# Performance work log

Hardware: AMD Instinct MI355X
Metric: run time of the kernel (lower is better)

Reference implementation:

```python
import jax, jax.numpy as jnp
import numpy as np
import math

B, S, D, H, R = 4, 2048, 2048, 16, 16
HD = D // H

def setup_inputs() -> dict:
    key = jax.random.key(0)
    ks = jax.random.split(key, 16)
    x = jax.random.normal(ks[0], (B, S, D), dtype=jnp.float32)
    # causal mask: 1 where attendable, 0 where masked (mask==0 -> -1e9)
    mask = jnp.tril(jnp.ones((S, S), dtype=jnp.int32))[None, None, :, :]
    def lin(k):
        return jax.random.normal(k, (D, D), dtype=jnp.float32) / math.sqrt(D)
    def lora(ka, kb):
        A = jax.random.normal(ka, (R, D), dtype=jnp.float32) / math.sqrt(D)
        Bm = jnp.zeros((D, R), dtype=jnp.float32)  # standard LoRA init: B = 0
        return A, Bm
    Aq, Bq = lora(ks[1], ks[2]); Ak, Bk = lora(ks[3], ks[4])
    Av, Bv = lora(ks[5], ks[6]); Ao, Bo = lora(ks[7], ks[8])
    return {"x": x, "mask": mask,
            "Wq": lin(ks[9]), "Aq": Aq, "Bq": Bq,
            "Wk": lin(ks[10]), "Ak": Ak, "Bk": Bk,
            "Wv": lin(ks[11]), "Av": Av, "Bv": Bv,
            "Wo": lin(ks[12]), "Ao": Ao, "Bo": Bo}

def _lora_linear(x, W, A, Bm):
    # y = x @ W^T + (x @ A^T) @ B^T   (LoRA-augmented linear, no bias)
    return x @ W.T + (x @ A.T) @ Bm.T

def reference(x, mask, Wq, Aq, Bq, Wk, Ak, Bk, Wv, Av, Bv, Wo, Ao, Bo):
    b, s, d = x.shape
    def heads(t):
        return t.reshape(b, s, H, HD).transpose(0, 2, 1, 3)  # [B,H,S,HD]
    Q = heads(_lora_linear(x, Wq, Aq, Bq))
    K = heads(_lora_linear(x, Wk, Ak, Bk))
    V = heads(_lora_linear(x, Wv, Av, Bv))
    attn = jnp.einsum('bhqd,bhkd->bhqk', Q, K) / math.sqrt(HD)
    attn = jnp.where(mask == 0, jnp.float32(-1e9), attn)
    attn = jax.nn.softmax(attn, axis=-1)
    out = jnp.einsum('bhqk,bhkd->bhqd', attn, V)  # [B,H,S,HD]
    out = out.transpose(0, 2, 1, 3).reshape(b, s, d)
    return _lora_linear(out, Wo, Ao, Bo)
```

## Files before the change

### kernel.cpp

```cpp
#include <hip/hip_runtime.h>
#include <hip/hip_bf16.h>
#include <stdint.h>


#define L2E 1.4426950408889634f
#define SMSCALE 0.08838834764831845f
#define NEGBIG -3.0e38f

typedef __attribute__((ext_vector_type(4))) float f32x4;
typedef __attribute__((ext_vector_type(16))) float f32x16;
typedef __attribute__((ext_vector_type(8))) __bf16 bfrag;

#if __has_builtin(__builtin_amdgcn_exp2f)
#define EXP2 __builtin_amdgcn_exp2f
#else
#define EXP2 exp2f
#endif

#define DRAIN_VM                                      \
  do {                                                \
    asm volatile("s_waitcnt vmcnt(0)" ::: "memory");  \
    __builtin_amdgcn_sched_barrier(0);                \
  } while (0)

static __device__ __forceinline__ unsigned short f2bf(float f) {
  union { float f; unsigned u; } v; v.f = f;
  unsigned r = v.u + 0x7FFFu + ((v.u >> 16) & 1u);
  return (unsigned short)(r >> 16);
}

static __device__ __forceinline__ void gload16(const void* g, void* l) {
  __builtin_amdgcn_global_load_lds(
      (const __attribute__((address_space(1))) void*)g,
      (__attribute__((address_space(3))) void*)l, 16, 0, 0);
}

__global__ __launch_bounds__(256) void k_fold(const float* __restrict__ W,
                                              const float* __restrict__ A,
                                              const float* __restrict__ Bm,
                                              unsigned short* __restrict__ out) {
  const int n = blockIdx.x;
  const int k0 = threadIdx.x * 8;
  const float* wr = W + (size_t)n * 2048 + k0;
  float acc[8];
#pragma unroll
  for (int j = 0; j < 8; ++j) acc[j] = wr[j];
#pragma unroll 4
  for (int r = 0; r < 16; ++r) {
    float b = Bm[n * 16 + r];
    const float* ar = A + (size_t)r * 2048 + k0;
#pragma unroll
    for (int j = 0; j < 8; ++j) acc[j] = fmaf(b, ar[j], acc[j]);
  }
  unsigned short o[8];
#pragma unroll
  for (int j = 0; j < 8; ++j) o[j] = f2bf(acc[j]);
  *(uint4*)(out + (size_t)n * 2048 + k0) = *(const uint4*)o;
}

__global__ __launch_bounds__(256) void k_cvt(const float* __restrict__ in,
                                             unsigned short* __restrict__ out) {
  const size_t i = ((size_t)blockIdx.x * 256 + threadIdx.x) * 8;
  unsigned short o[8];
#pragma unroll
  for (int j = 0; j < 8; ++j) o[j] = f2bf(in[i + j]);
  *(uint4*)(out + i) = *(const uint4*)o;
}

template <int MODE>
__global__ __launch_bounds__(512, 2) void k_gemm2(const unsigned short* __restrict__ A,
                                                  const unsigned short* __restrict__ Bw,
                                                  void* __restrict__ Cout, float scale) {
  __shared__ __align__(16) unsigned char lds[131072];
  unsigned char* Al = lds;
  unsigned char* Bl = lds + 65536;
  const int tid = threadIdx.x, ln = tid & 63;
  const int w = tid >> 6, g = ln >> 4, cc = ln & 15;
  const int wm = w >> 2, wn = w & 3;
  const int bid = blockIdx.x;
  const int wg = (bid & 7) * 32 + (bid >> 3);
  const int m0 = (wg >> 3) * 256, n0 = (wg & 7) * 256;

  int soff[2], sdst[2];
#pragma unroll
  for (int i = 0; i < 2; ++i) {
    int cid = i * 512 + tid, r = cid >> 2, p = cid & 3;
    int sc = p ^ ((r >> 1) & 3);
    soff[i] = r * 2048 + sc * 8;
    sdst[i] = cid * 16;
  }
  int aro[8], bro[4];
#pragma unroll
  for (int fm = 0; fm < 8; ++fm) {
    int r = wm * 128 + fm * 16 + cc;
    aro[fm] = r * 64 + ((g ^ ((r >> 1) & 3)) << 4);
  }
#pragma unroll
  for (int fn = 0; fn < 4; ++fn) {
    int r = wn * 64 + fn * 16 + cc;
    bro[fn] = r * 64 + ((g ^ ((r >> 1) & 3)) << 4);
  }

#define STAGE_A(b, kt, h)                                                   \
  do {                                                                      \
    _Pragma("unroll")                                                       \
    for (int i = 0; i < 2; ++i)                                             \
      gload16(A + (size_t)m0 * 2048 + soff[i] + (kt) + (h) * 32,            \
              Al + (b) * 32768 + (h) * 16384 + sdst[i]);                    \
  } while (0)
#define STAGE_B(b, kt, h)                                                   \
  do {                                                                      \
    _Pragma("unroll")                                                       \
    for (int i = 0; i < 2; ++i)                                             \
      gload16(Bw + (size_t)n0 * 2048 + soff[i] + (kt) + (h) * 32,           \
              Bl + (b) * 32768 + (h) * 16384 + sdst[i]);                    \
  } while (0)

  f32x4 acc[8][4] = {};

  STAGE_A(0, 0, 0); STAGE_B(0, 0, 0);
  STAGE_A(0, 0, 1); STAGE_B(0, 0, 1);
  STAGE_A(1, 64, 0); STAGE_B(1, 64, 0);
  asm volatile("s_waitcnt vmcnt(8)" ::: "memory");
  __builtin_amdgcn_s_barrier();
  __builtin_amdgcn_sched_barrier(0);

  for (int T = 0; T < 32; ++T) {
    const int buf = T & 1;
    const unsigned char* Ab = Al + buf * 32768;
    const unsigned char* Bb = Bl + buf * 32768;
#pragma unroll
    for (int ks = 0; ks < 2; ++ks) {
      bfrag af[8], bf[4];
#pragma unroll
      for (int fm = 0; fm < 8; ++fm)
        af[fm] = *(const bfrag*)(Ab + ks * 16384 + aro[fm]);
#pragma unroll
      for (int j = 0; j < 2; ++j)
        bf[j] = *(const bfrag*)(Bb + ks * 16384 + bro[j]);
      __builtin_amdgcn_sched_barrier(0);
      __builtin_amdgcn_s_barrier();
      __builtin_amdgcn_sched_barrier(0);
      __builtin_amdgcn_s_setprio(1);
#pragma unroll
      for (int fm = 0; fm < 8; ++fm)
#pragma unroll
        for (int j = 0; j < 2; ++j)
          acc[fm][j] = __builtin_amdgcn_mfma_f32_16x16x32_bf16(af[fm], bf[j],
                                                               acc[fm][j], 0, 0, 0);
      __builtin_amdgcn_s_setprio(0);
      __builtin_amdgcn_sched_barrier(0);
#pragma unroll
      for (int j = 0; j < 2; ++j)
        bf[2 + j] = *(const bfrag*)(Bb + ks * 16384 + bro[2 + j]);
      if (ks == 0) {
        if (T + 1 < 32) {
          STAGE_A(buf ^ 1, (T + 1) * 64, 1);
          STAGE_B(buf ^ 1, (T + 1) * 64, 1);
        }
        __builtin_amdgcn_sched_barrier(0);
        if (T < 31) asm volatile("s_waitcnt vmcnt(8)" ::: "memory");
        else        asm volatile("s_waitcnt vmcnt(0)" ::: "memory");
      } else {
        if (T + 2 < 32) {
          STAGE_A(buf, (T + 2) * 64, 0);
          STAGE_B(buf, (T + 2) * 64, 0);
        }
        __builtin_amdgcn_sched_barrier(0);
        if (T < 30) asm volatile("s_waitcnt vmcnt(8)" ::: "memory");
        else        asm volatile("s_waitcnt vmcnt(0)" ::: "memory");
      }
      __builtin_amdgcn_s_barrier();
      __builtin_amdgcn_sched_barrier(0);
      __builtin_amdgcn_s_setprio(1);
#pragma unroll
      for (int fm = 0; fm < 8; ++fm)
#pragma unroll
        for (int j = 0; j < 2; ++j)
          acc[fm][2 + j] = __builtin_amdgcn_mfma_f32_16x16x32_bf16(af[fm], bf[2 + j],
                                                                   acc[fm][2 + j], 0, 0, 0);
      __builtin_amdgcn_s_setprio(0);
      __builtin_amdgcn_sched_barrier(0);
    }
  }
#undef STAGE_A
#undef STAGE_B

#pragma unroll
  for (int fm = 0; fm < 8; ++fm)
#pragma unroll
    for (int fn = 0; fn < 4; ++fn)
#pragma unroll
      for (int r = 0; r < 4; ++r) {
        int row = m0 + wm * 128 + fm * 16 + g * 4 + r;
        int col = n0 + wn * 64 + fn * 16 + cc;
        float v = acc[fm][fn][r];
        if (MODE == 0) {
          int b = row >> 11, s = row & 2047, h = col >> 7, hd = col & 127;
          ((unsigned short*)Cout)[(((size_t)b * 16 + h) * 2048 + s) * 128 + hd] =
              f2bf(v * scale);
        } else if (MODE == 2) {
          int b = row >> 11, s = row & 2047, h = col >> 7, hd = col & 127;
          ((unsigned short*)Cout)[(((size_t)b * 16 + h) * 128 + hd) * 2048 + s] =
              f2bf(v);
        } else {
          ((float*)Cout)[(size_t)row * 2048 + col] = v;
        }
      }
}

__global__ __launch_bounds__(512) void k_attn(const unsigned short* __restrict__ Q,
                                              const unsigned short* __restrict__ K,
                                              const unsigned short* __restrict__ Vt,
                                              unsigned short* __restrict__ O) {
  __shared__ __align__(16) unsigned char lds[65536];
  const int tid = threadIdx.x;
  const int ln = tid & 63, w = tid >> 6;
  const int l31 = ln & 31, hi = ln >> 5;
  const int rk = l31 & 15;
  const int bx = blockIdx.x;
  const int qb = 7 - (bx >> 6);
  const int bh = bx & 63;
  const int q0 = qb * 256;
  const size_t base = (size_t)bh * 2048 * 128;
  const unsigned short* Qb = Q + base;
  const unsigned short* Kb = K + base;
  const unsigned short* Vb = Vt + base;

  const int qw0 = q0 + w * 32;
  const int qg = qw0 + l31;

  bfrag qf[8];
#pragma unroll
  for (int dc = 0; dc < 8; ++dc)
    qf[dc] = *(const bfrag*)(Qb + (size_t)qg * 128 + dc * 16 + hi * 8);

  f32x16 o[4] = {};
  float m_r = NEGBIG, l_r = 0.f;

  const int nt = q0 / 64 + 4;

  auto stage = [&](int buf, int k0) {
    unsigned char* Kt = lds + buf * 32768;
    unsigned char* Vl = Kt + 16384;
#pragma unroll
    for (int i = 0; i < 2; ++i) {
      int cid = i * 512 + tid;
      int row = cid >> 4, p = cid & 15, sc = p ^ (row & 15);
      gload16(Kb + (size_t)(k0 + row) * 128 + sc * 8, Kt + cid * 16);
    }
#pragma unroll
    for (int i = 0; i < 2; ++i) {
      int cid = i * 512 + tid;
      int row = cid >> 4, p = cid & 15, sc = p ^ (row & 15);
      int d = (sc >> 3) * 64 + row;
      gload16(Vb + (size_t)d * 2048 + k0 + (sc & 7) * 8, Vl + cid * 16);
    }
  };

  stage(0, 0);
  DRAIN_VM;
  __syncthreads();
  int buf = 0;

  for (int t = 0; t < nt; ++t) {
    const int k0 = t * 64;
    if (t + 1 < nt) stage(buf ^ 1, k0 + 64);

    if (k0 <= qw0 + 31) {
      const unsigned char* Kt = lds + buf * 32768;
      const unsigned char* Vl = Kt + 16384;

      f32x16 s0 = {}, s1 = {};
#pragma unroll
      for (int dc = 0; dc < 8; ++dc) {
        int c = dc * 2 + hi;
        bfrag ka = *(const bfrag*)(Kt + (size_t)l31 * 256 + ((c ^ rk) << 4));
        bfrag kb2 = *(const bfrag*)(Kt + (size_t)(32 + l31) * 256 + ((c ^ rk) << 4));
        s0 = __builtin_amdgcn_mfma_f32_32x32x16_bf16(ka, qf[dc], s0, 0, 0, 0);
        s1 = __builtin_amdgcn_mfma_f32_32x32x16_bf16(kb2, qf[dc], s1, 0, 0, 0);
      }

      if (k0 + 63 > qw0) {
#pragma unroll
        for (int r = 0; r < 16; ++r) {
          int ko = (r & 3) + 8 * (r >> 2) + 4 * hi;
          if (k0 + ko > qg) s0[r] = NEGBIG;
          if (k0 + 32 + ko > qg) s1[r] = NEGBIG;
        }
      }

      float pmax = s0[0];
#pragma unroll
      for (int r = 1; r < 16; ++r) pmax = fmaxf(pmax, s0[r]);
#pragma unroll
      for (int r = 0; r < 16; ++r) pmax = fmaxf(pmax, s1[r]);
      pmax = fmaxf(pmax, __shfl_xor(pmax, 32));

      if (!__all(pmax - m_r <= 12.f)) {
        float mn = fmaxf(m_r, pmax);
        float al = EXP2(m_r - mn);
        l_r *= al;
#pragma unroll
        for (int db = 0; db < 4; ++db)
#pragma unroll
          for (int r = 0; r < 16; ++r) o[db][r] *= al;
        m_r = mn;
      }

      unsigned qd0[8], qd1[8];
      float rs = 0.f;
#pragma unroll
      for (int s = 0; s < 4; ++s) {
        float p0 = EXP2(s0[4 * s + 0] - m_r), p1 = EXP2(s0[4 * s + 1] - m_r);
        float p2 = EXP2(s0[4 * s + 2] - m_r), p3 = EXP2(s0[4 * s + 3] - m_r);
        rs += (p0 + p1) + (p2 + p3);
        qd0[2 * s] = (unsigned)f2bf(p0) | ((unsigned)f2bf(p1) << 16);
        qd0[2 * s + 1] = (unsigned)f2bf(p2) | ((unsigned)f2bf(p3) << 16);
      }
#pragma unroll
      for (int s = 0; s < 4; ++s) {
        float p0 = EXP2(s1[4 * s + 0] - m_r), p1 = EXP2(s1[4 * s + 1] - m_r);
        float p2 = EXP2(s1[4 * s + 2] - m_r), p3 = EXP2(s1[4 * s + 3] - m_r);
        rs += (p0 + p1) + (p2 + p3);
        qd1[2 * s] = (unsigned)f2bf(p0) | ((unsigned)f2bf(p1) << 16);
        qd1[2 * s + 1] = (unsigned)f2bf(p2) | ((unsigned)f2bf(p3) << 16);
      }
      rs += __shfl_xor(rs, 32);
      l_r += rs;

#define PVSTEP(QD, B0, KC)                                                    \
  do {                                                                        \
    unsigned e0 = QD[B0], e1 = QD[B0 + 1], x0 = QD[B0 + 2], x1 = QD[B0 + 3];  \
    unsigned kp0 = hi ? x0 : e0, kp1 = hi ? x1 : e1;                          \
    unsigned sd0 = hi ? e0 : x0, sd1 = hi ? e1 : x1;                          \
    unsigned rc0 = (unsigned)__shfl_xor((int)sd0, 32);                        \
    unsigned rc1 = (unsigned)__shfl_xor((int)sd1, 32);                        \
    unsigned pw[4];                                                           \
    pw[0] = hi ? rc0 : kp0; pw[1] = hi ? rc1 : kp1;                           \
    pw[2] = hi ? kp0 : rc0; pw[3] = hi ? kp1 : rc1;                           \
    bfrag pf = *(bfrag*)pw;                                                   \
    _Pragma("unroll")                                                         \
    for (int db = 0; db < 4; ++db) {                                          \
      int c = (db >> 1) * 8 + KC * 2 + hi;                                    \
      bfrag vf = *(const bfrag*)(Vl + (size_t)((db & 1) * 32 + l31) * 256 +   \
                                 ((c ^ rk) << 4));                            \
      o[db] = __builtin_amdgcn_mfma_f32_32x32x16_bf16(vf, pf, o[db], 0, 0, 0);\
    }                                                                         \
  } while (0)

      PVSTEP(qd0, 0, 0);
      PVSTEP(qd0, 4, 1);
      PVSTEP(qd1, 0, 2);
      PVSTEP(qd1, 4, 3);
#undef PVSTEP
    }
    DRAIN_VM;
    __syncthreads();
    buf ^= 1;
  }

  float invl = 1.0f / l_r;
  const int b_ = bh >> 4, h_ = bh & 15;
#pragma unroll
  for (int ph = 0; ph < 2; ++ph) {
    if ((w >> 2) == ph) {
      unsigned char* ep = lds + (w & 3) * 8704;
#pragma unroll
      for (int db = 0; db < 4; ++db)
#pragma unroll
        for (int s = 0; s < 4; ++s) {
          int d0 = db * 32 + 8 * s + 4 * hi;
          float v0 = o[db][4 * s] * invl, v1 = o[db][4 * s + 1] * invl;
          float v2 = o[db][4 * s + 2] * invl, v3 = o[db][4 * s + 3] * invl;
          uint2 pw;
          pw.x = (unsigned)f2bf(v0) | ((unsigned)f2bf(v1) << 16);
          pw.y = (unsigned)f2bf(v2) | ((unsigned)f2bf(v3) << 16);
          *(uint2*)(ep + l31 * 272 + d0 * 2) = pw;
        }
    }
    __syncthreads();
    if ((w >> 2) == ph) {
      const unsigned char* ep = lds + (w & 3) * 8704;
#pragma unroll
      for (int i = 0; i < 8; ++i) {
        int cid = i * 64 + ln;
        int q = cid >> 4, ch = cid & 15;
        uint4 val = *(const uint4*)(ep + q * 272 + ch * 16);
        *(uint4*)(O + ((size_t)(b_ * 2048 + q0 + w * 32 + q)) * 2048 +
                  h_ * 128 + ch * 8) = val;
      }
    }
    __syncthreads();
  }
}

extern "C" void kernel_launch(void* const* d_in, const int* in_sizes, int n_in,
                              void* d_out, int out_size, void* d_ws, size_t ws_size,
                              hipStream_t stream) {
  (void)in_sizes; (void)n_in; (void)out_size; (void)ws_size;
  const float* x  = (const float*)d_in[0];
  const float* Wq = (const float*)d_in[2];
  const float* Aq = (const float*)d_in[3];
  const float* Bq = (const float*)d_in[4];
  const float* Wk = (const float*)d_in[5];
  const float* Ak = (const float*)d_in[6];
  const float* Bk = (const float*)d_in[7];
  const float* Wv = (const float*)d_in[8];
  const float* Av = (const float*)d_in[9];
  const float* Bv = (const float*)d_in[10];
  const float* Wo = (const float*)d_in[11];
  const float* Ao = (const float*)d_in[12];
  const float* Bo = (const float*)d_in[13];

  char* ws = (char*)d_ws;
  unsigned short* xbf = (unsigned short*)ws;
  unsigned short* Wqe = (unsigned short*)(ws + (size_t)33554432);
  unsigned short* Wke = Wqe + 2048 * 2048;
  unsigned short* Wve = Wke + 2048 * 2048;
  unsigned short* Woe = Wve + 2048 * 2048;
  unsigned short* Qb  = (unsigned short*)(ws + (size_t)33554432 + 4u * 8388608u);
  unsigned short* Kb  = Qb + 16777216;
  unsigned short* Vtb = Kb + 16777216;
  unsigned short* AO  = xbf;

  k_fold<<<2048, 256, 0, stream>>>(Wq, Aq, Bq, Wqe);
  k_fold<<<2048, 256, 0, stream>>>(Wk, Ak, Bk, Wke);
  k_fold<<<2048, 256, 0, stream>>>(Wv, Av, Bv, Wve);
  k_fold<<<2048, 256, 0, stream>>>(Wo, Ao, Bo, Woe);
  k_cvt<<<8192, 256, 0, stream>>>(x, xbf);

  k_gemm2<0><<<256, 512, 0, stream>>>(xbf, Wqe, Qb, SMSCALE * L2E);
  k_gemm2<0><<<256, 512, 0, stream>>>(xbf, Wke, Kb, 1.0f);
  k_gemm2<2><<<256, 512, 0, stream>>>(xbf, Wve, Vtb, 1.0f);

  k_attn<<<512, 512, 0, stream>>>(Qb, Kb, Vtb, AO);

  k_gemm2<1><<<256, 512, 0, stream>>>(AO, Woe, d_out, 1.0f);
}
```

Baseline: 411.2 us.

## Fuse QKV projections into one GEMM launch, batch weight folds, use 32x32 MFMA

Merges the four LoRA weight-fold launches into one 2D-grid launch and the three Q/K/V projection GEMMs into a single 768-block GEMM over a concatenated 6144-row weight matrix. The epilogue routes each output column segment to Q (scaled), K or transposed V. It also switches the inner product from 16x16x32 to 32x32x16 bf16 MFMA with new fragment addressing. The intent is to cut launch overhead and tail effects and raise MFMA efficiency. In exchange, the epilogue store pattern changes, with each lane now writing strided rows per register.

```diff
diff --git a/kernel.cpp b/kernel.cpp
--- a/kernel.cpp
+++ b/kernel.cpp
@@ -35,12 +35,19 @@
       (__attribute__((address_space(3))) void*)l, 16, 0, 0);
 }
 
-__global__ __launch_bounds__(256) void k_fold(const float* __restrict__ W,
-                                              const float* __restrict__ A,
-                                              const float* __restrict__ Bm,
-                                              unsigned short* __restrict__ out) {
+struct F4 {
+  const float* W[4];
+  const float* A[4];
+  const float* Bm[4];
+};
+
+__global__ __launch_bounds__(256) void k_fold4(F4 f, unsigned short* __restrict__ out) {
+  const int y = blockIdx.y;
   const int n = blockIdx.x;
   const int k0 = threadIdx.x * 8;
+  const float* W = f.W[y];
+  const float* Aa = f.A[y];
+  const float* Bm = f.Bm[y];
   const float* wr = W + (size_t)n * 2048 + k0;
   float acc[8];
 #pragma unroll
@@ -48,14 +55,14 @@
 #pragma unroll 4
   for (int r = 0; r < 16; ++r) {
     float b = Bm[n * 16 + r];
-    const float* ar = A + (size_t)r * 2048 + k0;
+    const float* ar = Aa + (size_t)r * 2048 + k0;
 #pragma unroll
     for (int j = 0; j < 8; ++j) acc[j] = fmaf(b, ar[j], acc[j]);
   }
   unsigned short o[8];
 #pragma unroll
   for (int j = 0; j < 8; ++j) o[j] = f2bf(acc[j]);
-  *(uint4*)(out + (size_t)n * 2048 + k0) = *(const uint4*)o;
+  *(uint4*)(out + (((size_t)y * 2048 + n) * 2048) + k0) = *(const uint4*)o;
 }
 
 __global__ __launch_bounds__(256) void k_cvt(const float* __restrict__ in,
@@ -67,19 +74,19 @@
   *(uint4*)(out + i) = *(const uint4*)o;
 }
 
-template <int MODE>
-__global__ __launch_bounds__(512, 2) void k_gemm2(const unsigned short* __restrict__ A,
+template <bool QKV>
+__global__ __launch_bounds__(512, 2) void k_gemm3(const unsigned short* __restrict__ A,
                                                   const unsigned short* __restrict__ Bw,
                                                   void* __restrict__ Cout, float scale) {
   __shared__ __align__(16) unsigned char lds[131072];
   unsigned char* Al = lds;
   unsigned char* Bl = lds + 65536;
   const int tid = threadIdx.x, ln = tid & 63;
-  const int w = tid >> 6, g = ln >> 4, cc = ln & 15;
+  const int w = tid >> 6, l31 = ln & 31, hi = ln >> 5;
   const int wm = w >> 2, wn = w & 3;
   const int bid = blockIdx.x;
-  const int wg = (bid & 7) * 32 + (bid >> 3);
-  const int m0 = (wg >> 3) * 256, n0 = (wg & 7) * 256;
+  const int wg = (bid & 7) * (QKV ? 96 : 32) + (bid >> 3);
+  const int m0 = (wg & 31) * 256, n0 = (wg >> 5) * 256;
 
   int soff[2], sdst[2];
 #pragma unroll
@@ -89,16 +96,16 @@
     soff[i] = r * 2048 + sc * 8;
     sdst[i] = cid * 16;
   }
-  int aro[8], bro[4];
-#pragma unroll
-  for (int fm = 0; fm < 8; ++fm) {
-    int r = wm * 128 + fm * 16 + cc;
-    aro[fm] = r * 64 + ((g ^ ((r >> 1) & 3)) << 4);
-  }
-#pragma unroll
-  for (int fn = 0; fn < 4; ++fn) {
-    int r = wn * 64 + fn * 16 + cc;
-    bro[fn] = r * 64 + ((g ^ ((r >> 1) & 3)) << 4);
+  int arow[4], axr[4], brow[2], bxr[2];
+#pragma unroll
+  for (int mt = 0; mt < 4; ++mt) {
+    int r = wm * 128 + mt * 32 + l31;
+    arow[mt] = r * 64; axr[mt] = (r >> 1) & 3;
+  }
+#pragma unroll
+  for (int nt = 0; nt < 2; ++nt) {
+    int r = wn * 64 + nt * 32 + l31;
+    brow[nt] = r * 64; bxr[nt] = (r >> 1) & 3;
   }
 
 #define STAGE_A(b, kt, h)                                                   \
@@ -116,7 +123,7 @@
               Bl + (b) * 32768 + (h) * 16384 + sdst[i]);                    \
   } while (0)
 
-  f32x4 acc[8][4] = {};
+  f32x16 acc[4][2] = {};
 
   STAGE_A(0, 0, 0); STAGE_B(0, 0, 0);
   STAGE_A(0, 0, 1); STAGE_B(0, 0, 1);
@@ -131,28 +138,33 @@
     const unsigned char* Bb = Bl + buf * 32768;
 #pragma unroll
     for (int ks = 0; ks < 2; ++ks) {
-      bfrag af[8], bf[4];
-#pragma unroll
-      for (int fm = 0; fm < 8; ++fm)
-        af[fm] = *(const bfrag*)(Ab + ks * 16384 + aro[fm]);
-#pragma unroll
-      for (int j = 0; j < 2; ++j)
-        bf[j] = *(const bfrag*)(Bb + ks * 16384 + bro[j]);
+      bfrag af[4][2], bf[2][2];
+#pragma unroll
+      for (int mt = 0; mt < 4; ++mt)
+#pragma unroll
+        for (int kk = 0; kk < 2; ++kk)
+          af[mt][kk] = *(const bfrag*)(Ab + ks * 16384 + arow[mt] +
+                                       ((((kk << 1) | hi) ^ axr[mt]) << 4));
+#pragma unroll
+      for (int kk = 0; kk < 2; ++kk)
+        bf[0][kk] = *(const bfrag*)(Bb + ks * 16384 + brow[0] +
+                                    ((((kk << 1) | hi) ^ bxr[0]) << 4));
       __builtin_amdgcn_sched_barrier(0);
       __builtin_amdgcn_s_barrier();
       __builtin_amdgcn_sched_barrier(0);
       __builtin_amdgcn_s_setprio(1);
 #pragma unroll
-      for (int fm = 0; fm < 8; ++fm)
-#pragma unroll
-        for (int j = 0; j < 2; ++j)
-          acc[fm][j] = __builtin_amdgcn_mfma_f32_16x16x32_bf16(af[fm], bf[j],
-                                                               acc[fm][j], 0, 0, 0);
+      for (int kk = 0; kk < 2; ++kk)
+#pragma unroll
+        for (int mt = 0; mt < 4; ++mt)
+          acc[mt][0] = __builtin_amdgcn_mfma_f32_32x32x16_bf16(af[mt][kk], bf[0][kk],
+                                                               acc[mt][0], 0, 0, 0);
       __builtin_amdgcn_s_setprio(0);
       __builtin_amdgcn_sched_barrier(0);
 #pragma unroll
-      for (int j = 0; j < 2; ++j)
-        bf[2 + j] = *(const bfrag*)(Bb + ks * 16384 + bro[2 + j]);
+      for (int kk = 0; kk < 2; ++kk)
+        bf[1][kk] = *(const bfrag*)(Bb + ks * 16384 + brow[1] +
+                                    ((((kk << 1) | hi) ^ bxr[1]) << 4));
       if (ks == 0) {
         if (T + 1 < 32) {
           STAGE_A(buf ^ 1, (T + 1) * 64, 1);
@@ -174,11 +186,11 @@
       __builtin_amdgcn_sched_barrier(0);
       __builtin_amdgcn_s_setprio(1);
 #pragma unroll
-      for (int fm = 0; fm < 8; ++fm)
-#pragma unroll
-        for (int j = 0; j < 2; ++j)
-          acc[fm][2 + j] = __builtin_amdgcn_mfma_f32_16x16x32_bf16(af[fm], bf[2 + j],
-                                                                   acc[fm][2 + j], 0, 0, 0);
+      for (int kk = 0; kk < 2; ++kk)
+#pragma unroll
+        for (int mt = 0; mt < 4; ++mt)
+          acc[mt][1] = __builtin_amdgcn_mfma_f32_32x32x16_bf16(af[mt][kk], bf[1][kk],
+                                                               acc[mt][1], 0, 0, 0);
       __builtin_amdgcn_s_setprio(0);
       __builtin_amdgcn_sched_barrier(0);
     }
@@ -186,23 +198,27 @@
 #undef STAGE_A
 #undef STAGE_B
 
-#pragma unroll
-  for (int fm = 0; fm < 8; ++fm)
-#pragma unroll
-    for (int fn = 0; fn < 4; ++fn)
-#pragma unroll
-      for (int r = 0; r < 4; ++r) {
-        int row = m0 + wm * 128 + fm * 16 + g * 4 + r;
-        int col = n0 + wn * 64 + fn * 16 + cc;
-        float v = acc[fm][fn][r];
-        if (MODE == 0) {
-          int b = row >> 11, s = row & 2047, h = col >> 7, hd = col & 127;
-          ((unsigned short*)Cout)[(((size_t)b * 16 + h) * 2048 + s) * 128 + hd] =
-              f2bf(v * scale);
-        } else if (MODE == 2) {
-          int b = row >> 11, s = row & 2047, h = col >> 7, hd = col & 127;
-          ((unsigned short*)Cout)[(((size_t)b * 16 + h) * 128 + hd) * 2048 + s] =
-              f2bf(v);
+  const int seg = QKV ? (n0 >> 11) : 1;
+  const float sc = (QKV && seg == 0) ? scale : 1.0f;
+#pragma unroll
+  for (int mt = 0; mt < 4; ++mt)
+#pragma unroll
+    for (int nt = 0; nt < 2; ++nt)
+#pragma unroll
+      for (int r = 0; r < 16; ++r) {
+        int row = m0 + wm * 128 + mt * 32 + (r & 3) + ((r >> 2) << 3) + (hi << 2);
+        int col = n0 + wn * 64 + nt * 32 + l31;
+        float v = acc[mt][nt][r];
+        if (QKV) {
+          int b = row >> 11, s = row & 2047;
+          int cs = col & 2047, h = cs >> 7, hd = cs & 127;
+          if (seg < 2) {
+            unsigned short* D = (unsigned short*)Cout + (size_t)seg * 16777216;
+            D[(((size_t)b * 16 + h) * 2048 + s) * 128 + hd] = f2bf(v * sc);
+          } else {
+            unsigned short* D = (unsigned short*)Cout + (size_t)2 * 16777216;
+            D[(((size_t)b * 16 + h) * 128 + hd) * 2048 + s] = f2bf(v);
+          }
         } else {
           ((float*)Cout)[(size_t)row * 2048 + col] = v;
         }
@@ -400,41 +416,27 @@
                               hipStream_t stream) {
   (void)in_sizes; (void)n_in; (void)out_size; (void)ws_size;
   const float* x  = (const float*)d_in[0];
-  const float* Wq = (const float*)d_in[2];
-  const float* Aq = (const float*)d_in[3];
-  const float* Bq = (const float*)d_in[4];
-  const float* Wk = (const float*)d_in[5];
-  const float* Ak = (const float*)d_in[6];
-  const float* Bk = (const float*)d_in[7];
-  const float* Wv = (const float*)d_in[8];
-  const float* Av = (const float*)d_in[9];
-  const float* Bv = (const float*)d_in[10];
-  const float* Wo = (const float*)d_in[11];
-  const float* Ao = (const float*)d_in[12];
-  const float* Bo = (const float*)d_in[13];
 
   char* ws = (char*)d_ws;
-  unsigned short* xbf = (unsigned short*)ws;
-  unsigned short* Wqe = (unsigned short*)(ws + (size_t)33554432);
-  unsigned short* Wke = Wqe + 2048 * 2048;
-  unsigned short* Wve = Wke + 2048 * 2048;
-  unsigned short* Woe = Wve + 2048 * 2048;
-  unsigned short* Qb  = (unsigned short*)(ws + (size_t)33554432 + 4u * 8388608u);
-  unsigned short* Kb  = Qb + 16777216;
-  unsigned short* Vtb = Kb + 16777216;
-  unsigned short* AO  = xbf;
-
-  k_fold<<<2048, 256, 0, stream>>>(Wq, Aq, Bq, Wqe);
-  k_fold<<<2048, 256, 0, stream>>>(Wk, Ak, Bk, Wke);
-  k_fold<<<2048, 256, 0, stream>>>(Wv, Av, Bv, Wve);
-  k_fold<<<2048, 256, 0, stream>>>(Wo, Ao, Bo, Woe);
+  unsigned short* xbf  = (unsigned short*)ws;
+  unsigned short* Wall = (unsigned short*)(ws + (size_t)33554432);
+  unsigned short* Qb   = (unsigned short*)(ws + (size_t)67108864);
+  unsigned short* Kb   = Qb + 16777216;
+  unsigned short* Vtb  = Kb + 16777216;
+  unsigned short* AO   = xbf;
+
+  F4 f;
+  f.W[0] = (const float*)d_in[2];  f.A[0] = (const float*)d_in[3];  f.Bm[0] = (const float*)d_in[4];
+  f.W[1] = (const float*)d_in[5];  f.A[1] = (const float*)d_in[6];  f.Bm[1] = (const float*)d_in[7];
+  f.W[2] = (const float*)d_in[8];  f.A[2] = (const float*)d_in[9];  f.Bm[2] = (const float*)d_in[10];
+  f.W[3] = (const float*)d_in[11]; f.A[3] = (const float*)d_in[12]; f.Bm[3] = (const float*)d_in[13];
+
+  k_fold4<<<dim3(2048, 4), 256, 0, stream>>>(f, Wall);
   k_cvt<<<8192, 256, 0, stream>>>(x, xbf);
 
-  k_gemm2<0><<<256, 512, 0, stream>>>(xbf, Wqe, Qb, SMSCALE * L2E);
-  k_gemm2<0><<<256, 512, 0, stream>>>(xbf, Wke, Kb, 1.0f);
-  k_gemm2<2><<<256, 512, 0, stream>>>(xbf, Wve, Vtb, 1.0f);
+  k_gemm3<true><<<768, 512, 0, stream>>>(xbf, Wall, Qb, SMSCALE * L2E);
 
   k_attn<<<512, 512, 0, stream>>>(Qb, Kb, Vtb, AO);
 
-  k_gemm2<1><<<256, 512, 0, stream>>>(AO, Woe, d_out, 1.0f);
-}
+  k_gemm3<false><<<256, 512, 0, stream>>>(AO, Wall + (size_t)6144 * 2048, d_out, 1.0f);
+}
```

Result: slower. 532.9 us (+29.6%).
